# Kernel tuning notes

Measured on AMD Instinct MI355X. Metric: run time of the kernel, lower is better.

The kernel has to match this reference:

```python
import jax, jax.numpy as jnp
import numpy as np

B, I, H, O = 4096, 1024, 2048, 1024


def _glorot(key, shape, fan_in):
    bound = 1.0 / np.sqrt(fan_in)
    return jax.random.uniform(key, shape, jnp.float32, -bound, bound)


def setup_inputs() -> dict:
    key = jax.random.key(0)
    ks = jax.random.split(key, 16)
    inp = {
        "x": jax.random.normal(ks[0], (B, I), jnp.float32),
        "hidden_state": jax.random.normal(ks[1], (B, H), jnp.float32),
        "cell_state": jax.random.normal(ks[2], (B, H), jnp.float32),
    }
    # Per-gate weights, torch nn.Linear convention: y = x @ W.T + b
    names = ["i", "f", "c", "o"]
    for n, (ka, kb, kc) in zip(names, zip(ks[3:7], ks[7:11], ks[11:15])):
        inp[f"Wx{n}_w"] = _glorot(ka, (H, I), I)
        inp[f"Wx{n}_b"] = _glorot(kb, (H,), I)
        inp[f"Wh{n}_w"] = _glorot(kc, (H, H), H)
    k1, k2 = jax.random.split(ks[15])
    inp["Why_w"] = _glorot(k1, (O, H), H)
    inp["Why_b"] = _glorot(k2, (O,), H)
    return inp


def reference(x, hidden_state, cell_state,
              Wxi_w, Wxi_b, Whi_w,
              Wxf_w, Wxf_b, Whf_w,
              Wxc_w, Wxc_b, Whc_w,
              Wxo_w, Wxo_b, Who_w,
              Why_w, Why_b):
    # Fuse the 8 small linears into one stacked GEMM per input: [B, I] @ [I, 4H]
    Wx = jnp.concatenate([Wxi_w, Wxf_w, Wxc_w, Wxo_w], axis=0)   # [4H, I]
    Wh = jnp.concatenate([Whi_w, Whf_w, Whc_w, Who_w], axis=0)   # [4H, H]
    bx = jnp.concatenate([Wxi_b, Wxf_b, Wxc_b, Wxo_b], axis=0)   # [4H]
    gates = x @ Wx.T + hidden_state @ Wh.T + bx                  # [B, 4H]
    gi, gf, gc, go = jnp.split(gates, 4, axis=-1)
    input_gate = jax.nn.sigmoid(gi)
    forget_gate = jax.nn.sigmoid(gf)
    cell_node = jnp.tanh(gc)
    output_gate = jax.nn.sigmoid(go)
    new_cell = forget_gate * cell_state + input_gate * cell_node
    new_hidden = output_gate * jnp.tanh(new_cell)
    output = new_hidden @ Why_w.T + Why_b
    return (output, new_hidden, new_cell)
```

## Files before the change

kernel.cpp:

```cpp
#include <hip/hip_runtime.h>
#include <hip/hip_bf16.h>

#define B_ 4096
#define I_ 1024
#define H_ 2048
#define O_ 1024
#define K1 (I_ + H_)
#define N1 (4 * H_)

typedef short v8s __attribute__((ext_vector_type(8)));
typedef float v4f __attribute__((ext_vector_type(4)));

__device__ __forceinline__ ushort f2bf(float f) {
    unsigned u = __float_as_uint(f);
    u += 0x7fffu + ((u >> 16) & 1u);
    return (ushort)(u >> 16);
}
__device__ __forceinline__ float sigm(float x) { return 1.f / (1.f + __expf(-x)); }
__device__ __forceinline__ float tanh_f(float x) {
    x = fminf(15.f, fmaxf(-15.f, x));
    float e = __expf(2.f * x);
    return (e - 1.f) / (e + 1.f);
}
__device__ __forceinline__ void gload16(const void* g, void* l) {
    __builtin_amdgcn_global_load_lds(
        (const __attribute__((address_space(1))) void*)g,
        (__attribute__((address_space(3))) void*)l, 16, 0, 0);
}
__device__ __forceinline__ void barrier_fenced() {
    __builtin_amdgcn_sched_barrier(0);
    asm volatile("" ::: "memory");
    __builtin_amdgcn_s_barrier();
    __builtin_amdgcn_sched_barrier(0);
    asm volatile("" ::: "memory");
}

__global__ __launch_bounds__(384) void convert_all(
    const float* __restrict__ Wxi, const float* __restrict__ Whi,
    const float* __restrict__ Wxf, const float* __restrict__ Whf,
    const float* __restrict__ Wxc, const float* __restrict__ Whc,
    const float* __restrict__ Wxo, const float* __restrict__ Who,
    const float* __restrict__ x,  const float* __restrict__ hs,
    const float* __restrict__ Why,
    ushort* __restrict__ Wcat, ushort* __restrict__ Xcat, ushort* __restrict__ WhyB)
{
    const int b = blockIdx.x;
    if (b < N1) {
        const int n = b, k = threadIdx.x * 8;
        const int h = n >> 2, g = n & 3;
        const float* src;
        if (k < I_) {
            const float* W = (g == 0) ? Wxi : (g == 1) ? Wxf : (g == 2) ? Wxc : Wxo;
            src = W + (size_t)h * I_ + k;
        } else {
            const float* W = (g == 0) ? Whi : (g == 1) ? Whf : (g == 2) ? Whc : Who;
            src = W + (size_t)h * H_ + (k - I_);
        }
        float4 a = *(const float4*)src;
        float4 c = *(const float4*)(src + 4);
        *(ushort4*)&Wcat[(size_t)n * K1 + k] =
            make_ushort4(f2bf(a.x), f2bf(a.y), f2bf(a.z), f2bf(a.w));
        *(ushort4*)&Wcat[(size_t)n * K1 + k + 4] =
            make_ushort4(f2bf(c.x), f2bf(c.y), f2bf(c.z), f2bf(c.w));
    } else if (b < N1 + B_) {
        const int m = b - N1, k = threadIdx.x * 8;
        const float* src = (k < I_) ? (x + (size_t)m * I_ + k)
                                    : (hs + (size_t)m * H_ + (k - I_));
        float4 a = *(const float4*)src;
        float4 c = *(const float4*)(src + 4);
        *(ushort4*)&Xcat[(size_t)m * K1 + k] =
            make_ushort4(f2bf(a.x), f2bf(a.y), f2bf(a.z), f2bf(a.w));
        *(ushort4*)&Xcat[(size_t)m * K1 + k + 4] =
            make_ushort4(f2bf(c.x), f2bf(c.y), f2bf(c.z), f2bf(c.w));
    } else {
        const int n = b - N1 - B_, k = threadIdx.x * 8;
        if (k < H_) {
            const float* src = Why + (size_t)n * H_ + k;
            float4 a = *(const float4*)src;
            float4 c = *(const float4*)(src + 4);
            *(ushort4*)&WhyB[(size_t)n * H_ + k] =
                make_ushort4(f2bf(a.x), f2bf(a.y), f2bf(a.z), f2bf(a.w));
            *(ushort4*)&WhyB[(size_t)n * H_ + k + 4] =
                make_ushort4(f2bf(c.x), f2bf(c.y), f2bf(c.z), f2bf(c.w));
        }
    }
}


#define STAGE(D, TT) {                                                        \
    const int kb_ = (TT) * 64;                                                \
    ushort* l0_ = (ushort*)lds + (D) * 16384 + tid * 8;                       \
    gload16(aSrc + kb_,             l0_);                                     \
    gload16(aSrc + 64 * K1 + kb_,   l0_ + 4096);                              \
    gload16(bSrc + kb_,             l0_ + 8192);                              \
    gload16(bSrc + 64 * K1 + kb_,   l0_ + 12288);                             \
}

#define COMPUTE(D) {                                                          \
    const ushort* ba_ = (const ushort*)lds + (D) * 16384 + aRowU;             \
    const ushort* bb_ = (const ushort*)lds + (D) * 16384 + 8192 + bRowU;      \
    v8s af_[4][2], bf_[2][2];                                                 \
    _Pragma("unroll")                                                         \
    for (int mi = 0; mi < 4; ++mi) {                                          \
        af_[mi][0] = *(const v8s*)&ba_[mi * 1024 + col0];                     \
        af_[mi][1] = *(const v8s*)&ba_[mi * 1024 + col1];                     \
    }                                                                         \
    _Pragma("unroll")                                                         \
    for (int ni = 0; ni < 2; ++ni) {                                          \
        bf_[ni][0] = *(const v8s*)&bb_[ni * 1024 + col0];                     \
        bf_[ni][1] = *(const v8s*)&bb_[ni * 1024 + col1];                     \
    }                                                                         \
    _Pragma("unroll")                                                         \
    for (int mi = 0; mi < 4; ++mi)                                            \
      _Pragma("unroll")                                                       \
      for (int ni = 0; ni < 2; ++ni) {                                        \
        acc[mi][ni] = __builtin_amdgcn_mfma_f32_16x16x32_bf16(                \
            af_[mi][0], bf_[ni][0], acc[mi][ni], 0, 0, 0);                    \
        acc[mi][ni] = __builtin_amdgcn_mfma_f32_16x16x32_bf16(                \
            af_[mi][1], bf_[ni][1], acc[mi][ni], 0, 0, 0);                    \
      }                                                                       \
}

__global__ __launch_bounds__(512, 4) void gates_mm_128w8(
    const ushort* __restrict__ A, const ushort* __restrict__ Bm,
    const float* __restrict__ cs,
    const float* __restrict__ bxi, const float* __restrict__ bxf,
    const float* __restrict__ bxc, const float* __restrict__ bxo,
    float* __restrict__ hid_out, float* __restrict__ cell_out,
    ushort* __restrict__ hidB)
{
    __shared__ ushort lds[32768];

    const int tid  = threadIdx.x;
    const int lane = tid & 63;
    const int w    = tid >> 6;
    const int wm = w >> 2;
    const int wn = w & 3;

    const int blkN = blockIdx.x;
    const int blkM = blockIdx.y;

    const int srowS = tid >> 3;
    const int colES = (((tid & 7) ^ (srowS & 7)) << 3);
    const ushort* aSrc = A  + (size_t)(blkM * 128 + srowS) * K1 + colES;
    const ushort* bSrc = Bm + (size_t)(blkN * 128 + srowS) * K1 + colES;

    const int l15 = lane & 15, l4 = lane >> 4;
    const int fx = l15 & 7;
    const int col0 = ((l4      ^ fx) << 3);
    const int col1 = (((4 + l4) ^ fx) << 3);
    const int aRowU = (wm * 64 + l15) * 64;
    const int bRowU = (wn * 32 + l15) * 64;

    v4f acc[4][2];
    #pragma unroll
    for (int mi = 0; mi < 4; ++mi)
      #pragma unroll
      for (int ni = 0; ni < 2; ++ni) acc[mi][ni] = (v4f)0.f;

    STAGE(0, 0)
    #pragma unroll 1
    for (int t = 0; t < 47; ++t) {
        STAGE((t + 1) & 1, t + 1)
        asm volatile("s_waitcnt vmcnt(4)" ::: "memory");
        barrier_fenced();
        COMPUTE(t & 1)
        barrier_fenced();
    }
    asm volatile("s_waitcnt vmcnt(0)" ::: "memory");
    barrier_fenced();
    COMPUTE(1)
    barrier_fenced();

    float*  csT = (float*)lds;
    float*  cT  = (float*)lds + 4352;
    float*  hT  = (float*)lds + 8704;
    ushort* hbT = (ushort*)lds + 26112;

    const int g = lane & 3;
    const int q = lane & 60;
    const int Mb = blkM * 128;
    const int hbase = blkN * 32;

    int hl[2]; float biasj[2];
    #pragma unroll
    for (int ni = 0; ni < 2; ++ni) {
        hl[ni] = wn * 8 + ni * 4 + (l15 >> 2);
        const float* bp = (g == 0) ? bxi : (g == 1) ? bxf : (g == 2) ? bxc : bxo;
        biasj[ni] = bp[hbase + hl[ni]];
    }

    const int erow = tid >> 2;
    const int ecol = (tid & 3) * 8;
    {
        const float* srcc = cs + (size_t)(Mb + erow) * H_ + hbase + ecol;
        *(float4*)&csT[erow * 34 + ecol]     = *(const float4*)(srcc);
        *(float4*)&csT[erow * 34 + ecol + 4] = *(const float4*)(srcc + 4);
    }
    __syncthreads();
    #pragma unroll
    for (int mi = 0; mi < 4; ++mi) {
      #pragma unroll
      for (int r = 0; r < 4; ++r) {
        const int ml = wm * 64 + mi * 16 + l4 * 4 + r;
        #pragma unroll
        for (int ni = 0; ni < 2; ++ni) {
            const float v = acc[mi][ni][r] + biasj[ni];
            const float gi = __shfl(v, q + 0, 64);
            const float gf = __shfl(v, q + 1, 64);
            const float gc = __shfl(v, q + 2, 64);
            const float go = __shfl(v, q + 3, 64);
            const float Ig = sigm(gi), Fg = sigm(gf);
            const float Cg = tanh_f(gc), Og = sigm(go);
            const float c_old = csT[ml * 34 + hl[ni]];
            const float c_new = Fg * c_old + Ig * Cg;
            const float h_new = Og * tanh_f(c_new);
            if (g == 0)      cT [ml * 34 + hl[ni]] = c_new;
            else if (g == 1) hT [ml * 34 + hl[ni]] = h_new;
            else if (g == 2) hbT[ml * 36 + hl[ni]] = f2bf(h_new);
        }
      }
    }
    __syncthreads();
    {
        const size_t gof = (size_t)(Mb + erow) * H_ + hbase + ecol;
        *(float4*)&cell_out[gof]     = *(const float4*)&cT[erow * 34 + ecol];
        *(float4*)&cell_out[gof + 4] = *(const float4*)&cT[erow * 34 + ecol + 4];
        *(float4*)&hid_out [gof]     = *(const float4*)&hT[erow * 34 + ecol];
        *(float4*)&hid_out [gof + 4] = *(const float4*)&hT[erow * 34 + ecol + 4];
        *(uint2*)&hidB[gof]          = *(const uint2*)&hbT[erow * 36 + ecol];
        *(uint2*)&hidB[gof + 4]      = *(const uint2*)&hbT[erow * 36 + ecol + 4];
    }
}

__global__ __launch_bounds__(256) void out_mm_bf16(
    const ushort* __restrict__ A, const ushort* __restrict__ Bm,
    const float* __restrict__ bw, float* __restrict__ out)
{
    __shared__ ushort As[128 * 32];
    __shared__ ushort Bs[128 * 32];
    const int tid  = threadIdx.x;
    const int lane = tid & 63;
    const int w    = tid >> 6;
    const int wm = w >> 1, wn = w & 1;
    const int blkN = blockIdx.x, blkM = blockIdx.y;
    const int srow = w * 16 + (lane >> 2);
    const int scol = (lane & 3) * 8;

    v4f acc[4][4];
    #pragma unroll
    for (int i = 0; i < 4; ++i)
      #pragma unroll
      for (int j = 0; j < 4; ++j) acc[i][j] = (v4f)0.f;

    for (int k0 = 0; k0 < H_; k0 += 32) {
        #pragma unroll
        for (int it = 0; it < 2; ++it) {
            const int row = it * 64 + srow;
            gload16(A  + (size_t)(blkM * 128 + row) * H_ + k0 + scol,
                    &As[w * 512 + it * 2048]);
            gload16(Bm + (size_t)(blkN * 128 + row) * H_ + k0 + scol,
                    &Bs[w * 512 + it * 2048]);
        }
        __syncthreads();
        v8s afr[4], bfr[4];
        #pragma unroll
        for (int i = 0; i < 4; ++i)
            afr[i] = *(const v8s*)&As[(wm * 64 + i * 16 + (lane & 15)) * 32 + (lane >> 4) * 8];
        #pragma unroll
        for (int j = 0; j < 4; ++j)
            bfr[j] = *(const v8s*)&Bs[(wn * 64 + j * 16 + (lane & 15)) * 32 + (lane >> 4) * 8];
        #pragma unroll
        for (int i = 0; i < 4; ++i)
          #pragma unroll
          for (int j = 0; j < 4; ++j)
            acc[i][j] = __builtin_amdgcn_mfma_f32_16x16x32_bf16(afr[i], bfr[j], acc[i][j], 0, 0, 0);
        __syncthreads();
    }
    #pragma unroll
    for (int i = 0; i < 4; ++i) {
      #pragma unroll
      for (int r = 0; r < 4; ++r) {
        const int m = blkM * 128 + wm * 64 + i * 16 + (lane >> 4) * 4 + r;
        #pragma unroll
        for (int j = 0; j < 4; ++j) {
            const int n = blkN * 128 + wn * 64 + j * 16 + (lane & 15);
            out[(size_t)m * O_ + n] = acc[i][j][r] + bw[n];
        }
      }
    }
}

extern "C" void kernel_launch(void* const* d_in, const int* in_sizes, int n_in,
                              void* d_out, int out_size, void* d_ws, size_t ws_size,
                              hipStream_t stream) {
    const float* x   = (const float*)d_in[0];
    const float* hs  = (const float*)d_in[1];
    const float* cs  = (const float*)d_in[2];
    const float* Wxi = (const float*)d_in[3];
    const float* bxi = (const float*)d_in[4];
    const float* Whi = (const float*)d_in[5];
    const float* Wxf = (const float*)d_in[6];
    const float* bxf = (const float*)d_in[7];
    const float* Whf = (const float*)d_in[8];
    const float* Wxc = (const float*)d_in[9];
    const float* bxc = (const float*)d_in[10];
    const float* Whc = (const float*)d_in[11];
    const float* Wxo = (const float*)d_in[12];
    const float* bxo = (const float*)d_in[13];
    const float* Who = (const float*)d_in[14];
    const float* Why = (const float*)d_in[15];
    const float* bwy = (const float*)d_in[16];

    float* out      = (float*)d_out;
    float* hid_out  = out + (size_t)B_ * O_;
    float* cell_out = hid_out + (size_t)B_ * H_;

    const size_t szW = (size_t)N1 * K1;
    const size_t szX = (size_t)B_ * K1;
    const size_t szY = (size_t)O_ * H_;

    ushort* Wcat = (ushort*)d_ws;
    ushort* Xcat = Wcat + szW;
    ushort* WhyB = Xcat + szX;
    ushort* HidB = WhyB + szY;

    convert_all<<<dim3(N1 + B_ + O_), 384, 0, stream>>>(
        Wxi, Whi, Wxf, Whf, Wxc, Whc, Wxo, Who, x, hs, Why, Wcat, Xcat, WhyB);

    gates_mm_128w8<<<dim3(N1 / 128, B_ / 128), 512, 0, stream>>>(
        Xcat, Wcat, cs, bxi, bxf, bxc, bxo, hid_out, cell_out, HidB);
    out_mm_bf16<<<dim3(O_ / 128, B_ / 128), 256, 0, stream>>>(
        HidB, WhyB, bwy, out);
}
```

Baseline: 348.7 us.

## Rewrite output GEMM with double-buffered swizzled LDS pipeline and MFMA priority

The output projection GEMM is rebuilt to match the gates kernel: 512 threads, a 128x128 tile with K-step 64, a swizzled LDS layout, and double buffering so global loads of the next K tile overlap MFMA compute on the current one. In addition, s_setprio is raised around the MFMA block inside COMPUTE, which affects both GEMMs. The aim is to hide global-load latency and reduce LDS bank conflicts in the second GEMM. Costs are more LDS per block and the barrier pattern that comes with the deeper pipeline.

New measurement: 344.8 us. Within noise of the previous version (-1.1%).

```diff
diff --git a/kernel.cpp b/kernel.cpp
--- a/kernel.cpp
+++ b/kernel.cpp
@@ -110,6 +110,7 @@
         bf_[ni][0] = *(const v8s*)&bb_[ni * 1024 + col0];                     \
         bf_[ni][1] = *(const v8s*)&bb_[ni * 1024 + col1];                     \
     }                                                                         \
+    __builtin_amdgcn_s_setprio(1);                                            \
     _Pragma("unroll")                                                         \
     for (int mi = 0; mi < 4; ++mi)                                            \
       _Pragma("unroll")                                                       \
@@ -119,6 +120,7 @@
         acc[mi][ni] = __builtin_amdgcn_mfma_f32_16x16x32_bf16(                \
             af_[mi][1], bf_[ni][1], acc[mi][ni], 0, 0, 0);                    \
       }                                                                       \
+    __builtin_amdgcn_s_setprio(0);                                            \
 }
 
 __global__ __launch_bounds__(512, 4) void gates_mm_128w8(
@@ -233,59 +235,71 @@
     }
 }
 
-__global__ __launch_bounds__(256) void out_mm_bf16(
+
+#define STAGE2(D, TT) {                                                       \
+    const int kb_ = (TT) * 64;                                                \
+    ushort* l0_ = (ushort*)lds + (D) * 16384 + tid * 8;                       \
+    gload16(aSrc + kb_,             l0_);                                     \
+    gload16(aSrc + 64 * H_ + kb_,   l0_ + 4096);                              \
+    gload16(bSrc + kb_,             l0_ + 8192);                              \
+    gload16(bSrc + 64 * H_ + kb_,   l0_ + 12288);                             \
+}
+
+__global__ __launch_bounds__(512, 4) void out_mm_bf16(
     const ushort* __restrict__ A, const ushort* __restrict__ Bm,
     const float* __restrict__ bw, float* __restrict__ out)
 {
-    __shared__ ushort As[128 * 32];
-    __shared__ ushort Bs[128 * 32];
+    __shared__ ushort lds[32768];
+
     const int tid  = threadIdx.x;
     const int lane = tid & 63;
     const int w    = tid >> 6;
-    const int wm = w >> 1, wn = w & 1;
-    const int blkN = blockIdx.x, blkM = blockIdx.y;
-    const int srow = w * 16 + (lane >> 2);
-    const int scol = (lane & 3) * 8;
-
-    v4f acc[4][4];
-    #pragma unroll
-    for (int i = 0; i < 4; ++i)
+    const int wm = w >> 2;
+    const int wn = w & 3;
+
+    const int blkN = blockIdx.x;
+    const int blkM = blockIdx.y;
+
+    const int srowS = tid >> 3;
+    const int colES = (((tid & 7) ^ (srowS & 7)) << 3);
+    const ushort* aSrc = A  + (size_t)(blkM * 128 + srowS) * H_ + colES;
+    const ushort* bSrc = Bm + (size_t)(blkN * 128 + srowS) * H_ + colES;
+
+    const int l15 = lane & 15, l4 = lane >> 4;
+    const int fx = l15 & 7;
+    const int col0 = ((l4      ^ fx) << 3);
+    const int col1 = (((4 + l4) ^ fx) << 3);
+    const int aRowU = (wm * 64 + l15) * 64;
+    const int bRowU = (wn * 32 + l15) * 64;
+
+    v4f acc[4][2];
+    #pragma unroll
+    for (int mi = 0; mi < 4; ++mi)
       #pragma unroll
-      for (int j = 0; j < 4; ++j) acc[i][j] = (v4f)0.f;
-
-    for (int k0 = 0; k0 < H_; k0 += 32) {
-        #pragma unroll
-        for (int it = 0; it < 2; ++it) {
-            const int row = it * 64 + srow;
-            gload16(A  + (size_t)(blkM * 128 + row) * H_ + k0 + scol,
-                    &As[w * 512 + it * 2048]);
-            gload16(Bm + (size_t)(blkN * 128 + row) * H_ + k0 + scol,
-                    &Bs[w * 512 + it * 2048]);
-        }
-        __syncthreads();
-        v8s afr[4], bfr[4];
-        #pragma unroll
-        for (int i = 0; i < 4; ++i)
-            afr[i] = *(const v8s*)&As[(wm * 64 + i * 16 + (lane & 15)) * 32 + (lane >> 4) * 8];
-        #pragma unroll
-        for (int j = 0; j < 4; ++j)
-            bfr[j] = *(const v8s*)&Bs[(wn * 64 + j * 16 + (lane & 15)) * 32 + (lane >> 4) * 8];
-        #pragma unroll
-        for (int i = 0; i < 4; ++i)
-          #pragma unroll
-          for (int j = 0; j < 4; ++j)
-            acc[i][j] = __builtin_amdgcn_mfma_f32_16x16x32_bf16(afr[i], bfr[j], acc[i][j], 0, 0, 0);
-        __syncthreads();
-    }
-    #pragma unroll
-    for (int i = 0; i < 4; ++i) {
+      for (int ni = 0; ni < 2; ++ni) acc[mi][ni] = (v4f)0.f;
+
+    STAGE2(0, 0)
+    #pragma unroll 1
+    for (int t = 0; t < 31; ++t) {
+        STAGE2((t + 1) & 1, t + 1)
+        asm volatile("s_waitcnt vmcnt(4)" ::: "memory");
+        barrier_fenced();
+        COMPUTE(t & 1)
+        barrier_fenced();
+    }
+    asm volatile("s_waitcnt vmcnt(0)" ::: "memory");
+    barrier_fenced();
+    COMPUTE(1)
+
+    #pragma unroll
+    for (int mi = 0; mi < 4; ++mi) {
       #pragma unroll
       for (int r = 0; r < 4; ++r) {
-        const int m = blkM * 128 + wm * 64 + i * 16 + (lane >> 4) * 4 + r;
+        const int m = blkM * 128 + wm * 64 + mi * 16 + l4 * 4 + r;
         #pragma unroll
-        for (int j = 0; j < 4; ++j) {
-            const int n = blkN * 128 + wn * 64 + j * 16 + (lane & 15);
-            out[(size_t)m * O_ + n] = acc[i][j][r] + bw[n];
+        for (int ni = 0; ni < 2; ++ni) {
+            const int n = blkN * 128 + wn * 32 + ni * 16 + l15;
+            out[(size_t)m * O_ + n] = acc[mi][ni][r] + bw[n];
         }
       }
     }
@@ -330,6 +344,6 @@
 
     gates_mm_128w8<<<dim3(N1 / 128, B_ / 128), 512, 0, stream>>>(
         Xcat, Wcat, cs, bxi, bxf, bxc, bxo, hid_out, cell_out, HidB);
-    out_mm_bf16<<<dim3(O_ / 128, B_ / 128), 256, 0, stream>>>(
+    out_mm_bf16<<<dim3(O_ / 128, B_ / 128), 512, 0, stream>>>(
         HidB, WhyB, bwy, out);
 }
```
